# Kernel tuning notes

Hardware: AMD Instinct MI355X
Metric: run time of the kernel (lower is better)

Reference implementation:

```python
import jax, jax.numpy as jnp
import numpy as np

VOCAB = 100
EMB = 256
HID = 256
B = 8
S = 2048


def setup_inputs() -> dict:
    key = jax.random.key(0)
    ks = jax.random.split(key, 12)
    s_e = 1.0 / np.sqrt(EMB)
    s_h = 1.0 / np.sqrt(HID)
    return {
        "x": jax.random.randint(ks[0], (B, S), 0, VOCAB),
        "embedding": jax.random.normal(ks[1], (VOCAB, EMB), jnp.float32),
        "w_ih": jax.random.uniform(ks[2], (3 * HID, EMB), jnp.float32, -s_e, s_e),
        "w_hh": jax.random.uniform(ks[3], (3 * HID, HID), jnp.float32, -s_h, s_h),
        "b_ih": jax.random.uniform(ks[4], (3 * HID,), jnp.float32, -s_h, s_h),
        "b_hh": jax.random.uniform(ks[5], (3 * HID,), jnp.float32, -s_h, s_h),
        "attn_w": jax.random.uniform(ks[6], (HID, HID), jnp.float32, -s_h, s_h),
        "attn_b": jax.random.uniform(ks[7], (HID,), jnp.float32, -s_h, s_h),
        "comb_w": jax.random.uniform(ks[8], (HID, 2 * HID), jnp.float32, -s_h, s_h),
        "comb_b": jax.random.uniform(ks[9], (HID,), jnp.float32, -s_h, s_h),
        "fc_w": jax.random.uniform(ks[10], (VOCAB, HID), jnp.float32, -s_h, s_h),
        "fc_b": jax.random.uniform(ks[11], (VOCAB,), jnp.float32, -s_h, s_h),
    }


def _gru(emb, w_ih, w_hh, b_ih, b_hh):
    # emb: [B, S, E]; PyTorch GRU gate order: r, z, n
    xg = jnp.einsum('bse,ge->bsg', emb, w_ih) + b_ih  # [B, S, 3H]
    h0 = jnp.zeros((emb.shape[0], HID), emb.dtype)

    def step(h, xg_t):
        hg = h @ w_hh.T + b_hh
        xr, xz, xn = jnp.split(xg_t, 3, axis=-1)
        hr, hz, hn = jnp.split(hg, 3, axis=-1)
        r = jax.nn.sigmoid(xr + hr)
        z = jax.nn.sigmoid(xz + hz)
        n = jnp.tanh(xn + r * hn)
        h_new = (1.0 - z) * n + z * h
        return h_new, h_new

    h_last, hs = jax.lax.scan(step, h0, jnp.swapaxes(xg, 0, 1))
    return jnp.swapaxes(hs, 0, 1), h_last  # [B,S,H], [B,H]


def reference(x, embedding, w_ih, w_hh, b_ih, b_hh, attn_w, attn_b, comb_w, comb_b, fc_w, fc_b):
    emb = embedding[x]  # [B, S, E]
    all_h, h_last = _gru(emb, w_ih, w_hh, b_ih, b_hh)
    keys = jnp.einsum('bsh,kh->bsk', all_h, attn_w) + attn_b  # [B,S,H]
    scores = jnp.einsum('bqh,bkh->bqk', all_h, keys)  # [B,S,S]
    seq = all_h.shape[1]
    causal = jnp.tril(jnp.ones((seq, seq), bool))
    scores = jnp.where(causal[None], scores, -jnp.inf)
    attn = jax.nn.softmax(scores, axis=-1)
    context = jnp.einsum('bqk,bkh->bqh', attn, all_h)  # [B,S,H]
    combined = jnp.concatenate([all_h, context], axis=-1)
    combined = jnp.tanh(jnp.einsum('bsd,hd->bsh', combined, comb_w) + comb_b)
    output = jnp.einsum('bsh,vh->bsv', combined, fc_w) + fc_b
    return output, h_last[None]  # hidden: [num_layers=1, B, H]
```

## Files before the change

kernel.cpp:

```cpp
#include <hip/hip_runtime.h>

#define SEQ  2048
#define NB   8
#define HD   256
#define G3   768
#define NV   100

typedef float f32x4 __attribute__((ext_vector_type(4)));
typedef int   i32x4 __attribute__((ext_vector_type(4)));
typedef short s16x8 __attribute__((ext_vector_type(8)));
typedef unsigned short u16x4 __attribute__((ext_vector_type(4)));

#define INV26 1.490116119384765625e-8f

__device__ __forceinline__ float rcp_fast(float x) {
  return __builtin_amdgcn_rcpf(x);
}
__device__ __forceinline__ float sigm(float x) {
  x = fminf(fmaxf(x, -30.f), 30.f);
  return rcp_fast(1.f + __expf(-x));
}
__device__ __forceinline__ float tanh_fast(float x) {
  x = fminf(fmaxf(x, -15.f), 15.f);
  float e = __expf(2.f * x);
  return (e - 1.f) * rcp_fast(e + 1.f);
}
__device__ __forceinline__ void cvt_hilo(float f, unsigned short& h, unsigned short& l) {
  unsigned u = __float_as_uint(f);
  h = (unsigned short)(u >> 16);
  float r = f - __uint_as_float(u & 0xffff0000u);
  l = (unsigned short)(__float_as_uint(r) >> 16);
}

__global__ __launch_bounds__(256) void build_table(
    const float* __restrict__ emb, const float* __restrict__ w_ih,
    const float* __restrict__ b_ih, float* __restrict__ table) {
  __shared__ float eL[256];
  __shared__ float wL[256][37];
  int v = blockIdx.x, tid = threadIdx.x;
  eL[tid] = emb[v * HD + tid];
  for (int gt = 0; gt < 3; ++gt) {
    float acc = b_ih[gt * 256 + tid];
    for (int e0 = 0; e0 < HD; e0 += 32) {
      __syncthreads();
      #pragma unroll
      for (int i = 0; i < 32; ++i) {
        int idx = tid + i * 256;
        int r = idx >> 5, c = idx & 31;
        wL[r][c] = w_ih[(size_t)(gt * 256 + r) * HD + e0 + c];
      }
      __syncthreads();
      #pragma unroll
      for (int c = 0; c < 32; ++c) acc += eL[e0 + c] * wL[tid][c];
    }
    table[((size_t)v * 256 + tid) * 4 + gt] = acc;
  }
}

__global__ void __launch_bounds__(512) gru_scan(
    const int* __restrict__ x, const float* __restrict__ w_hh,
    const float* __restrict__ b_hh, const float* __restrict__ table,
    float* __restrict__ all_h, float* __restrict__ h_last) {
  __shared__ __align__(16) signed char hpk[2][2 * 272];
  __shared__ int xs[SEQ];
  const int b = blockIdx.x;
  int tid = threadIdx.x;
  int lane = tid & 63, wv = tid >> 6;
  int ncol = lane & 15, quad = lane >> 4;
  int usel = quad & 1;
  int j = wv * 32 + usel * 16 + ncol;

  for (int i = tid; i < SEQ; i += 512) xs[i] = x[b * SEQ + i];
  for (int i = tid; i < 2 * 272; i += 512)
    hpk[0][i] = (i >= 272) ? (signed char)-128 : 0;

  i32x4 bw[2][3][4];
  float Cn2[2][3];
  #pragma unroll
  for (int u = 0; u < 2; ++u) {
    #pragma unroll
    for (int t3 = 0; t3 < 3; ++t3) {
      int row = t3 * 256 + wv * 32 + u * 16 + ncol;
      int sw = 0;
      #pragma unroll
      for (int c = 0; c < 4; ++c) {
        const float* p = w_hh + (size_t)row * HD + c * 64 + quad * 16;
        unsigned pw[4] = {0u, 0u, 0u, 0u};
        #pragma unroll
        for (int e = 0; e < 16; ++e) {
          int q = __float2int_rn(p[e] * 2048.f);
          q = max(-127, min(127, q));
          sw += q;
          pw[e >> 2] |= ((unsigned)(q & 255)) << ((e & 3) * 8);
        }
        bw[u][t3][c] = (i32x4){(int)pw[0], (int)pw[1], (int)pw[2], (int)pw[3]};
      }
      sw += __shfl_xor(sw, 16);
      sw += __shfl_xor(sw, 32);
      Cn2[u][t3] = b_hh[row] + 128.f * (float)sw * INV26;
    }
  }
  float Csel[3];
  #pragma unroll
  for (int t3 = 0; t3 < 3; ++t3) Csel[t3] = usel ? Cn2[1][t3] : Cn2[0][t3];

  float hreg = 0.f;
  __syncthreads();
  float xr, xz, xn;
  {
    int v = xs[0];
    f32x4 xg = *(const f32x4*)&table[((size_t)v * 256 + j) * 4];
    xr = xg[0]; xz = xg[1]; xn = xg[2];
  }
  int a_base = (ncol & 1) * 272 + quad * 16;

  for (int t = 0; t < SEQ; ++t) {
    const signed char* cb = hpk[t & 1];
    i32x4 a[4];
    #pragma unroll
    for (int c = 0; c < 4; ++c)
      a[c] = *(const i32x4*)&cb[a_base + c * 64];
    float hg[3];
    #pragma unroll
    for (int t3 = 0; t3 < 3; ++t3) {
      i32x4 A0 = {0, 0, 0, 0}, A1 = {0, 0, 0, 0};
      #pragma unroll
      for (int c = 0; c < 4; ++c) {
        A0 = __builtin_amdgcn_mfma_i32_16x16x64_i8(a[c], bw[0][t3][c], A0, 0, 0, 0);
        A1 = __builtin_amdgcn_mfma_i32_16x16x64_i8(a[c], bw[1][t3][c], A1, 0, 0, 0);
      }
      int d0 = usel ? A1[0] : A0[0];
      int d1 = usel ? A1[1] : A0[1];
      hg[t3] = ((float)d0 * 256.f + (float)d1) * INV26 + Csel[t3];
    }
    float r = sigm(xr + hg[0]);
    float z = sigm(xz + hg[1]);
    float n = tanh_fast(xn + r * hg[2]);
    float h = (1.f - z) * n + z * hreg;
    hreg = h;
    int q = min(__float2int_rn(h * 32768.f), 32767);
    int lou = q & 255;
    int hi8 = (q - lou) >> 8;
    signed char* nx = hpk[(t + 1) & 1];
    if (quad < 2) {
      nx[j] = (signed char)hi8;
      nx[272 + j] = (signed char)(lou - 128);
      all_h[((size_t)b * SEQ + t) * HD + j] = h;
    }
    int v = xs[(t + 1 < SEQ) ? t + 1 : t];
    f32x4 xg = *(const f32x4*)&table[((size_t)v * 256 + j) * 4];
    xr = xg[0]; xz = xg[1]; xn = xg[2];
    __syncthreads();
  }
  if (quad < 2) h_last[b * HD + j] = hreg;
}

template<int ACT>
__global__ __launch_bounds__(256) void gemm_bias(
    const float* __restrict__ A, int lda,
    const float* __restrict__ W, const float* __restrict__ bias,
    float* __restrict__ C, int ldc, int N, int K) {
  __shared__ float As[128][36];
  __shared__ float Ws[64][36];
  int tid = threadIdx.x;
  int m0 = blockIdx.y * 128, n0 = blockIdx.x * 64;
  int ml = tid & 31, g = tid >> 5;
  float acc[4][8];
  #pragma unroll
  for (int i = 0; i < 4; ++i)
    #pragma unroll
    for (int jj = 0; jj < 8; ++jj) acc[i][jj] = 0.f;
  for (int k0 = 0; k0 < K; k0 += 32) {
    __syncthreads();
    #pragma unroll
    for (int i = 0; i < 4; ++i) {
      int idx = tid + i * 256;
      int r = idx >> 3, c4 = (idx & 7) * 4;
      *(f32x4*)&As[r][c4] = *(const f32x4*)&A[(size_t)(m0 + r) * lda + k0 + c4];
    }
    #pragma unroll
    for (int i = 0; i < 2; ++i) {
      int idx = tid + i * 256;
      int r = idx >> 3, c4 = (idx & 7) * 4;
      f32x4 wv = {0.f, 0.f, 0.f, 0.f};
      if (n0 + r < N) wv = *(const f32x4*)&W[(size_t)(n0 + r) * K + k0 + c4];
      *(f32x4*)&Ws[r][c4] = wv;
    }
    __syncthreads();
    #pragma unroll
    for (int k4 = 0; k4 < 32; k4 += 4) {
      f32x4 av[4], wv8[8];
      #pragma unroll
      for (int i = 0; i < 4; ++i) av[i] = *(const f32x4*)&As[ml + i * 32][k4];
      #pragma unroll
      for (int jj = 0; jj < 8; ++jj) wv8[jj] = *(const f32x4*)&Ws[g * 8 + jj][k4];
      #pragma unroll
      for (int kk = 0; kk < 4; ++kk)
        #pragma unroll
        for (int i = 0; i < 4; ++i)
          #pragma unroll
          for (int jj = 0; jj < 8; ++jj)
            acc[i][jj] += av[i][kk] * wv8[jj][kk];
    }
  }
  #pragma unroll
  for (int i = 0; i < 4; ++i) {
    int m = m0 + ml + i * 32;
    #pragma unroll
    for (int jj = 0; jj < 8; ++jj) {
      int n = n0 + g * 8 + jj;
      if (n < N) {
        float val = acc[i][jj] + bias[n];
        if (ACT) val = tanh_fast(val);
        C[(size_t)m * ldc + n] = val;
      }
    }
  }
}

__global__ __launch_bounds__(256) void gemm_bias_cat(
    const float* __restrict__ A1, const float* __restrict__ A2,
    const float* __restrict__ W, const float* __restrict__ bias,
    float* __restrict__ C) {
  __shared__ float As[128][36];
  __shared__ float Ws[64][36];
  const int K = 512;
  int tid = threadIdx.x;
  int m0 = blockIdx.y * 128, n0 = blockIdx.x * 64;
  int ml = tid & 31, g = tid >> 5;
  float acc[4][8];
  #pragma unroll
  for (int i = 0; i < 4; ++i)
    #pragma unroll
    for (int jj = 0; jj < 8; ++jj) acc[i][jj] = 0.f;
  for (int k0 = 0; k0 < K; k0 += 32) {
    const float* src = (k0 < 256) ? A1 : A2;
    int kb = (k0 < 256) ? k0 : k0 - 256;
    __syncthreads();
    #pragma unroll
    for (int i = 0; i < 4; ++i) {
      int idx = tid + i * 256;
      int r = idx >> 3, c4 = (idx & 7) * 4;
      *(f32x4*)&As[r][c4] = *(const f32x4*)&src[(size_t)(m0 + r) * 256 + kb + c4];
    }
    #pragma unroll
    for (int i = 0; i < 2; ++i) {
      int idx = tid + i * 256;
      int r = idx >> 3, c4 = (idx & 7) * 4;
      *(f32x4*)&Ws[r][c4] = *(const f32x4*)&W[(size_t)(n0 + r) * K + k0 + c4];
    }
    __syncthreads();
    #pragma unroll
    for (int k4 = 0; k4 < 32; k4 += 4) {
      f32x4 av[4], wv8[8];
      #pragma unroll
      for (int i = 0; i < 4; ++i) av[i] = *(const f32x4*)&As[ml + i * 32][k4];
      #pragma unroll
      for (int jj = 0; jj < 8; ++jj) wv8[jj] = *(const f32x4*)&Ws[g * 8 + jj][k4];
      #pragma unroll
      for (int kk = 0; kk < 4; ++kk)
        #pragma unroll
        for (int i = 0; i < 4; ++i)
          #pragma unroll
          for (int jj = 0; jj < 8; ++jj)
            acc[i][jj] += av[i][kk] * wv8[jj][kk];
    }
  }
  #pragma unroll
  for (int i = 0; i < 4; ++i) {
    int m = m0 + ml + i * 32;
    #pragma unroll
    for (int jj = 0; jj < 8; ++jj) {
      int n = n0 + g * 8 + jj;
      C[(size_t)m * 256 + n] = tanh_fast(acc[i][jj] + bias[n]);
    }
  }
}

__global__ __launch_bounds__(256, 1) void attention_kernel(
    const float* __restrict__ all_h, const float* __restrict__ keys,
    float* __restrict__ ctxg) {
  __shared__ __align__(16) unsigned short Khi[16][264], Klo[16][264];
  __shared__ __align__(16) unsigned short Vhi[256][24], Vlo[256][24];
  __shared__ __align__(16) unsigned short Pb[4][2][16][24];
  const int b = blockIdx.y, qb = blockIdx.x;
  int tid = threadIdx.x, lane = tid & 63, wv = tid >> 6;
  int lm = lane & 15, kg = lane >> 4;
  const float* hb = all_h + (size_t)b * SEQ * HD;
  const float* kb = keys  + (size_t)b * SEQ * HD;
  const int q0 = qb * 64 + wv * 16;

  s16x8 Qh[8], Ql[8];
  {
    const float* qp = hb + (size_t)(q0 + lm) * HD;
    #pragma unroll
    for (int ch = 0; ch < 8; ++ch) {
      union { s16x8 v; unsigned short u[8]; } uh, ul;
      f32x4 a0 = *(const f32x4*)&qp[ch * 32 + kg * 8];
      f32x4 a1 = *(const f32x4*)&qp[ch * 32 + kg * 8 + 4];
      #pragma unroll
      for (int e = 0; e < 4; ++e) {
        cvt_hilo(a0[e], uh.u[e], ul.u[e]);
        cvt_hilo(a1[e], uh.u[4 + e], ul.u[4 + e]);
      }
      Qh[ch] = uh.v; Ql[ch] = ul.v;
    }
  }

  f32x4 co[16];
  #pragma unroll
  for (int ht = 0; ht < 16; ++ht) co[ht] = (f32x4){0.f, 0.f, 0.f, 0.f};
  float mo[4] = {-3e38f, -3e38f, -3e38f, -3e38f};
  float lr[4] = {0.f, 0.f, 0.f, 0.f};

  const int nkt = 4 * qb + 4;
  for (int kt = 0; kt < nkt; ++kt) {
    int k0 = kt * 16;
    __syncthreads();
    #pragma unroll
    for (int i = 0; i < 4; ++i) {
      int idx = tid + i * 256;
      int r = idx & 15, cg = idx >> 4;
      f32x4 kv = *(const f32x4*)&kb[(size_t)(k0 + r) * HD + cg * 4];
      f32x4 vv = *(const f32x4*)&hb[(size_t)(k0 + r) * HD + cg * 4];
      u16x4 khv, klv;
      #pragma unroll
      for (int e = 0; e < 4; ++e) {
        unsigned short h16, l16;
        cvt_hilo(kv[e], h16, l16);
        khv[e] = h16; klv[e] = l16;
      }
      *(u16x4*)&Khi[r][cg * 4] = khv;
      *(u16x4*)&Klo[r][cg * 4] = klv;
      #pragma unroll
      for (int e = 0; e < 4; ++e) {
        unsigned short h16, l16;
        cvt_hilo(vv[e], h16, l16);
        Vhi[cg * 4 + e][r] = h16;
        Vlo[cg * 4 + e][r] = l16;
      }
    }
    __syncthreads();

    f32x4 acc[6];
    #pragma unroll
    for (int i = 0; i < 6; ++i) acc[i] = (f32x4){0.f, 0.f, 0.f, 0.f};
    #pragma unroll
    for (int ch = 0; ch < 8; ++ch) {
      s16x8 bh = *(const s16x8*)&Khi[lm][ch * 32 + kg * 8];
      s16x8 bl = *(const s16x8*)&Klo[lm][ch * 32 + kg * 8];
      int a = (ch & 1) * 3;
      acc[a + 0] = __builtin_amdgcn_mfma_f32_16x16x32_bf16(Qh[ch], bh, acc[a + 0], 0, 0, 0);
      acc[a + 1] = __builtin_amdgcn_mfma_f32_16x16x32_bf16(Ql[ch], bh, acc[a + 1], 0, 0, 0);
      acc[a + 2] = __builtin_amdgcn_mfma_f32_16x16x32_bf16(Qh[ch], bl, acc[a + 2], 0, 0, 0);
    }
    float p[4], al[4];
    #pragma unroll
    for (int r = 0; r < 4; ++r) {
      float s = acc[0][r] + acc[1][r] + acc[2][r] + acc[3][r] + acc[4][r] + acc[5][r];
      int valid = (k0 + lm) <= (q0 + kg * 4 + r);
      float t = valid ? s : -3e38f;
      t = fmaxf(t, __shfl_xor(t, 1));
      t = fmaxf(t, __shfl_xor(t, 2));
      t = fmaxf(t, __shfl_xor(t, 4));
      t = fmaxf(t, __shfl_xor(t, 8));
      float mn = fmaxf(mo[r], t);
      al[r] = __expf(mo[r] - mn);
      float pv = valid ? __expf(s - mn) : 0.f;
      p[r] = pv;
      float rs = pv;
      rs += __shfl_xor(rs, 1);
      rs += __shfl_xor(rs, 2);
      rs += __shfl_xor(rs, 4);
      rs += __shfl_xor(rs, 8);
      lr[r] = lr[r] * al[r] + rs;
      mo[r] = mn;
    }
    #pragma unroll
    for (int r = 0; r < 4; ++r) {
      unsigned short ph, pl;
      cvt_hilo(p[r], ph, pl);
      Pb[wv][0][kg * 4 + r][lm] = ph;
      Pb[wv][1][kg * 4 + r][lm] = pl;
    }
    s16x8 pah = {0, 0, 0, 0, 0, 0, 0, 0}, pal = {0, 0, 0, 0, 0, 0, 0, 0};
    if (kg < 2) {
      pah = *(const s16x8*)&Pb[wv][0][lm][kg * 8];
      pal = *(const s16x8*)&Pb[wv][1][lm][kg * 8];
    }
    #pragma unroll
    for (int ht = 0; ht < 16; ++ht) {
      f32x4 c = co[ht];
      #pragma unroll
      for (int r = 0; r < 4; ++r) c[r] *= al[r];
      s16x8 vh = {0, 0, 0, 0, 0, 0, 0, 0}, vl = {0, 0, 0, 0, 0, 0, 0, 0};
      if (kg < 2) {
        vh = *(const s16x8*)&Vhi[ht * 16 + lm][kg * 8];
        vl = *(const s16x8*)&Vlo[ht * 16 + lm][kg * 8];
      }
      c = __builtin_amdgcn_mfma_f32_16x16x32_bf16(pah, vh, c, 0, 0, 0);
      c = __builtin_amdgcn_mfma_f32_16x16x32_bf16(pah, vl, c, 0, 0, 0);
      c = __builtin_amdgcn_mfma_f32_16x16x32_bf16(pal, vh, c, 0, 0, 0);
      co[ht] = c;
    }
  }
  float li[4];
  #pragma unroll
  for (int r = 0; r < 4; ++r) li[r] = rcp_fast(lr[r]);
  #pragma unroll
  for (int ht = 0; ht < 16; ++ht)
    #pragma unroll
    for (int r = 0; r < 4; ++r)
      ctxg[((size_t)b * SEQ + q0 + kg * 4 + r) * HD + ht * 16 + lm] = co[ht][r] * li[r];
}

extern "C" void kernel_launch(void* const* d_in, const int* in_sizes, int n_in,
                              void* d_out, int out_size, void* d_ws, size_t ws_size,
                              hipStream_t stream) {
  (void)in_sizes; (void)n_in; (void)out_size; (void)ws_size;
  const int*   x      = (const int*)  d_in[0];
  const float* emb    = (const float*)d_in[1];
  const float* w_ih   = (const float*)d_in[2];
  const float* w_hh   = (const float*)d_in[3];
  const float* b_ih   = (const float*)d_in[4];
  const float* b_hh   = (const float*)d_in[5];
  const float* attn_w = (const float*)d_in[6];
  const float* attn_b = (const float*)d_in[7];
  const float* comb_w = (const float*)d_in[8];
  const float* comb_b = (const float*)d_in[9];
  const float* fc_w   = (const float*)d_in[10];
  const float* fc_b   = (const float*)d_in[11];
  float* out = (float*)d_out;

  float* ws    = (float*)d_ws;
  float* table = ws;
  float* all_h = table + 102400;
  float* keys  = all_h + 4194304;
  float* ctx   = keys  + 4194304;
  float* hlast = out + (size_t)NB * SEQ * NV;

  build_table<<<100, 256, 0, stream>>>(emb, w_ih, b_ih, table);
  gru_scan<<<NB, 512, 0, stream>>>(x, w_hh, b_hh, table, all_h, hlast);
  gemm_bias<0><<<dim3(4, 128), 256, 0, stream>>>(all_h, 256, attn_w, attn_b, keys, 256, 256, 256);
  attention_kernel<<<dim3(32, 8), 256, 0, stream>>>(all_h, keys, ctx);
  gemm_bias_cat<<<dim3(4, 128), 256, 0, stream>>>(all_h, ctx, comb_w, comb_b, keys);
  gemm_bias<0><<<dim3(2, 128), 256, 0, stream>>>(keys, 256, fc_w, fc_b, out, 100, 100, 256);
}
```

Baseline: 2.064 ms.

## Widen attention KV tile to 32 keys and swizzle LDS for MFMA fragments

The attention kernel now processes 32 keys per iteration instead of 16, so the P·V MFMA uses its full 32-wide K dimension instead of zero-padding half the lanes. K, V and P are stored in LDS in a fragment-major layout, so each lane loads its 8-element operand with one contiguous vector read. This halves the number of tile iterations and their barriers, and removes the half-wasted PV matrix ops. The cost is more LDS per block and more register pressure from the two score groups, plus more masked work on the diagonal tiles.

```diff
diff --git a/kernel.cpp b/kernel.cpp
--- a/kernel.cpp
+++ b/kernel.cpp
@@ -5,6 +5,7 @@
 #define HD   256
 #define G3   768
 #define NV   100
+#define KVB  32
 
 typedef float f32x4 __attribute__((ext_vector_type(4)));
 typedef int   i32x4 __attribute__((ext_vector_type(4)));
@@ -280,9 +281,9 @@
 __global__ __launch_bounds__(256, 1) void attention_kernel(
     const float* __restrict__ all_h, const float* __restrict__ keys,
     float* __restrict__ ctxg) {
-  __shared__ __align__(16) unsigned short Khi[16][264], Klo[16][264];
-  __shared__ __align__(16) unsigned short Vhi[256][24], Vlo[256][24];
-  __shared__ __align__(16) unsigned short Pb[4][2][16][24];
+  __shared__ __align__(16) unsigned short KH[2][8][516], KL[2][8][516];
+  __shared__ __align__(16) unsigned short VH[16][516], VL[16][516];
+  __shared__ __align__(16) unsigned short PB[4][2][520];
   const int b = blockIdx.y, qb = blockIdx.x;
   int tid = threadIdx.x, lane = tid & 63, wv = tid >> 6;
   int lm = lane & 15, kg = lane >> 4;
@@ -313,16 +314,16 @@
   float mo[4] = {-3e38f, -3e38f, -3e38f, -3e38f};
   float lr[4] = {0.f, 0.f, 0.f, 0.f};
 
-  const int nkt = 4 * qb + 4;
+  const int nkt = 2 * qb + 2;
   for (int kt = 0; kt < nkt; ++kt) {
-    int k0 = kt * 16;
-    __syncthreads();
-    #pragma unroll
-    for (int i = 0; i < 4; ++i) {
+    int k0 = kt * KVB;
+    __syncthreads();
+    #pragma unroll
+    for (int i = 0; i < 8; ++i) {
       int idx = tid + i * 256;
-      int r = idx & 15, cg = idx >> 4;
-      f32x4 kv = *(const f32x4*)&kb[(size_t)(k0 + r) * HD + cg * 4];
-      f32x4 vv = *(const f32x4*)&hb[(size_t)(k0 + r) * HD + cg * 4];
+      int r = idx >> 6, c = idx & 63;
+      f32x4 kv = *(const f32x4*)&kb[(size_t)(k0 + r) * HD + c * 4];
+      f32x4 vv = *(const f32x4*)&hb[(size_t)(k0 + r) * HD + c * 4];
       u16x4 khv, klv;
       #pragma unroll
       for (int e = 0; e < 4; ++e) {
@@ -330,45 +331,54 @@
         cvt_hilo(kv[e], h16, l16);
         khv[e] = h16; klv[e] = l16;
       }
-      *(u16x4*)&Khi[r][cg * 4] = khv;
-      *(u16x4*)&Klo[r][cg * 4] = klv;
+      int ch = c >> 3, kgs = (c & 7) >> 1;
+      int off = (kgs * 16 + (r & 15)) * 8 + (c & 1) * 4;
+      *(u16x4*)&KH[r >> 4][ch][off] = khv;
+      *(u16x4*)&KL[r >> 4][ch][off] = klv;
+      int kgv = r >> 3, ev = r & 7, ht = c >> 2;
       #pragma unroll
       for (int e = 0; e < 4; ++e) {
         unsigned short h16, l16;
         cvt_hilo(vv[e], h16, l16);
-        Vhi[cg * 4 + e][r] = h16;
-        Vlo[cg * 4 + e][r] = l16;
-      }
-    }
-    __syncthreads();
-
-    f32x4 acc[6];
-    #pragma unroll
-    for (int i = 0; i < 6; ++i) acc[i] = (f32x4){0.f, 0.f, 0.f, 0.f};
-    #pragma unroll
-    for (int ch = 0; ch < 8; ++ch) {
-      s16x8 bh = *(const s16x8*)&Khi[lm][ch * 32 + kg * 8];
-      s16x8 bl = *(const s16x8*)&Klo[lm][ch * 32 + kg * 8];
-      int a = (ch & 1) * 3;
-      acc[a + 0] = __builtin_amdgcn_mfma_f32_16x16x32_bf16(Qh[ch], bh, acc[a + 0], 0, 0, 0);
-      acc[a + 1] = __builtin_amdgcn_mfma_f32_16x16x32_bf16(Ql[ch], bh, acc[a + 1], 0, 0, 0);
-      acc[a + 2] = __builtin_amdgcn_mfma_f32_16x16x32_bf16(Qh[ch], bl, acc[a + 2], 0, 0, 0);
-    }
-    float p[4], al[4];
+        int o = (kgv * 16 + (c & 3) * 4 + e) * 8 + ev;
+        VH[ht][o] = h16; VL[ht][o] = l16;
+      }
+    }
+    __syncthreads();
+
+    float s[4][2];
+    #pragma unroll
+    for (int g = 0; g < 2; ++g) {
+      f32x4 a0 = {0.f,0.f,0.f,0.f}, a1 = {0.f,0.f,0.f,0.f}, a2 = {0.f,0.f,0.f,0.f};
+      #pragma unroll
+      for (int ch = 0; ch < 8; ++ch) {
+        s16x8 bh = *(const s16x8*)&KH[g][ch][lane * 8];
+        s16x8 bl = *(const s16x8*)&KL[g][ch][lane * 8];
+        a0 = __builtin_amdgcn_mfma_f32_16x16x32_bf16(Qh[ch], bh, a0, 0, 0, 0);
+        a1 = __builtin_amdgcn_mfma_f32_16x16x32_bf16(Ql[ch], bh, a1, 0, 0, 0);
+        a2 = __builtin_amdgcn_mfma_f32_16x16x32_bf16(Qh[ch], bl, a2, 0, 0, 0);
+      }
+      #pragma unroll
+      for (int r = 0; r < 4; ++r) s[r][g] = a0[r] + a1[r] + a2[r];
+    }
+    float p[4][2], al[4];
     #pragma unroll
     for (int r = 0; r < 4; ++r) {
-      float s = acc[0][r] + acc[1][r] + acc[2][r] + acc[3][r] + acc[4][r] + acc[5][r];
-      int valid = (k0 + lm) <= (q0 + kg * 4 + r);
-      float t = valid ? s : -3e38f;
+      int qrow = q0 + kg * 4 + r;
+      int va = (k0 + lm) <= qrow, vb = (k0 + 16 + lm) <= qrow;
+      float ta = va ? s[r][0] : -3e38f;
+      float tb = vb ? s[r][1] : -3e38f;
+      float t = fmaxf(ta, tb);
       t = fmaxf(t, __shfl_xor(t, 1));
       t = fmaxf(t, __shfl_xor(t, 2));
       t = fmaxf(t, __shfl_xor(t, 4));
       t = fmaxf(t, __shfl_xor(t, 8));
       float mn = fmaxf(mo[r], t);
       al[r] = __expf(mo[r] - mn);
-      float pv = valid ? __expf(s - mn) : 0.f;
-      p[r] = pv;
-      float rs = pv;
+      float pa = va ? __expf(s[r][0] - mn) : 0.f;
+      float pb = vb ? __expf(s[r][1] - mn) : 0.f;
+      p[r][0] = pa; p[r][1] = pb;
+      float rs = pa + pb;
       rs += __shfl_xor(rs, 1);
       rs += __shfl_xor(rs, 2);
       rs += __shfl_xor(rs, 4);
@@ -377,27 +387,25 @@
       mo[r] = mn;
     }
     #pragma unroll
-    for (int r = 0; r < 4; ++r) {
-      unsigned short ph, pl;
-      cvt_hilo(p[r], ph, pl);
-      Pb[wv][0][kg * 4 + r][lm] = ph;
-      Pb[wv][1][kg * 4 + r][lm] = pl;
-    }
-    s16x8 pah = {0, 0, 0, 0, 0, 0, 0, 0}, pal = {0, 0, 0, 0, 0, 0, 0, 0};
-    if (kg < 2) {
-      pah = *(const s16x8*)&Pb[wv][0][lm][kg * 8];
-      pal = *(const s16x8*)&Pb[wv][1][lm][kg * 8];
-    }
+    for (int r = 0; r < 4; ++r)
+      #pragma unroll
+      for (int g = 0; g < 2; ++g) {
+        unsigned short ph, pl;
+        cvt_hilo(p[r][g], ph, pl);
+        int key = g * 16 + lm;
+        int o = ((key >> 3) * 16 + kg * 4 + r) * 8 + (key & 7);
+        PB[wv][0][o] = ph;
+        PB[wv][1][o] = pl;
+      }
+    s16x8 pah = *(const s16x8*)&PB[wv][0][lane * 8];
+    s16x8 pal = *(const s16x8*)&PB[wv][1][lane * 8];
     #pragma unroll
     for (int ht = 0; ht < 16; ++ht) {
       f32x4 c = co[ht];
       #pragma unroll
       for (int r = 0; r < 4; ++r) c[r] *= al[r];
-      s16x8 vh = {0, 0, 0, 0, 0, 0, 0, 0}, vl = {0, 0, 0, 0, 0, 0, 0, 0};
-      if (kg < 2) {
-        vh = *(const s16x8*)&Vhi[ht * 16 + lm][kg * 8];
-        vl = *(const s16x8*)&Vlo[ht * 16 + lm][kg * 8];
-      }
+      s16x8 vh = *(const s16x8*)&VH[ht][lane * 8];
+      s16x8 vl = *(const s16x8*)&VL[ht][lane * 8];
       c = __builtin_amdgcn_mfma_f32_16x16x32_bf16(pah, vh, c, 0, 0, 0);
       c = __builtin_amdgcn_mfma_f32_16x16x32_bf16(pah, vl, c, 0, 0, 0);
       c = __builtin_amdgcn_mfma_f32_16x16x32_bf16(pal, vh, c, 0, 0, 0);
```

Result: faster. 1.954 ms (-5.3%).
